# Optimization experiments

Measured on AMD Instinct MI355X. Metric: run time of the kernel, lower is better.

The kernel has to match this reference:

```python
import jax, jax.numpy as jnp
import numpy as np

HEADS = 8
DIM_HEAD = 64
BOTTLENECK = 40


def setup_inputs() -> dict:
    key = jax.random.key(0)
    ks = jax.random.split(key, 10)
    b, n, qs = 4, 1024, 256
    inner = HEADS * DIM_HEAD
    s = lambda fan_in: 1.0 / np.sqrt(fan_in)
    return {
        "x":   jax.random.normal(ks[0], (b, n, qs), dtype=jnp.float32),
        # weights stored as (in, out) so forward is x @ W
        "wq1": jax.random.normal(ks[1], (qs, BOTTLENECK), dtype=jnp.float32) * s(qs),
        "wq2": jax.random.normal(ks[2], (BOTTLENECK, inner), dtype=jnp.float32) * s(BOTTLENECK),
        "wk1": jax.random.normal(ks[3], (qs, BOTTLENECK), dtype=jnp.float32) * s(qs),
        "wk2": jax.random.normal(ks[4], (BOTTLENECK, inner), dtype=jnp.float32) * s(BOTTLENECK),
        "wv1": jax.random.normal(ks[5], (qs, BOTTLENECK), dtype=jnp.float32) * s(qs),
        "wv2": jax.random.normal(ks[6], (BOTTLENECK, inner), dtype=jnp.float32) * s(BOTTLENECK),
        "wo":  jax.random.normal(ks[7], (inner, qs), dtype=jnp.float32) * s(inner),
        "bo":  jax.random.normal(ks[8], (qs,), dtype=jnp.float32) * 0.01,
    }


def reference(x, wq1, wq2, wk1, wk2, wv1, wv2, wo, bo):
    b, n, _ = x.shape
    h, d = HEADS, DIM_HEAD
    scale = d ** -0.5

    # bottlenecked QKV projections (40-dim), SiLU on K bottleneck
    q = (x @ wq1) @ wq2                       # (b, n, h*d)
    k = jax.nn.silu(x @ wk1) @ wk2            # (b, n, h*d)
    v = (x @ wv1) @ wv2                       # (b, n, h*d)

    def split(t):  # 'b n (h d) -> b (h n) d'
        return t.reshape(b, n, h, d).transpose(0, 2, 1, 3).reshape(b, h * n, d)

    q, k, v = split(q), split(k), split(v)

    sim = jnp.einsum('bid,bjd->bij', q, k) * scale   # (b, h*n, h*n)
    attn = jax.nn.softmax(sim, axis=-1)
    out = jnp.einsum('bij,bjd->bid', attn, v)        # (b, h*n, d)

    # 'b (h n) d -> b n (h d)'
    out = out.reshape(b, h, n, d).transpose(0, 2, 1, 3).reshape(b, n, h * d)
    return out @ wo + bo
```

## Files before the change

### kernel.cpp

```cpp
#include <hip/hip_runtime.h>
#include <hip/hip_bf16.h>


#define B_    4
#define H_    8
#define NSEQ  1024
#define SEQ   8192
#define DH    64
#define QS    256
#define INNER 512
#define QSCALE 0.18033688011112042f

#define KVSW_BATCH 524288

typedef __bf16 bf16x8 __attribute__((ext_vector_type(8)));
typedef float floatx4 __attribute__((ext_vector_type(4)));

__global__ __launch_bounds__(1024) void qkv_kernel(
    const float* __restrict__ x,
    const float* __restrict__ wq1, const float* __restrict__ wq2,
    const float* __restrict__ wk1, const float* __restrict__ wk2,
    const float* __restrict__ wv1, const float* __restrict__ wv2,
    __hip_bfloat16* __restrict__ Qg, __hip_bfloat16* __restrict__ KSg,
    __hip_bfloat16* __restrict__ VSg)
{
  const int tid  = threadIdx.x;
  const int b    = blockIdx.x >> 6;
  const int nblk = blockIdx.x & 63;
  const int n0   = nblk << 4;

  __shared__ __align__(16) float xs[16][260];
  __shared__ __align__(16) float tb2[2][3][16][40];
  __shared__ __align__(16) float tb[3][16][40];
  __shared__ __align__(16) __hip_bfloat16 qb[16][520];
  __shared__ __align__(16) __hip_bfloat16 kb[16][520];
  __shared__ __align__(16) __hip_bfloat16 vb[512][20];

  for (int i = tid; i < 16 * 256; i += 1024) {
    const int r = i >> 8, c = i & 255;
    xs[r][c] = x[((size_t)b * NSEQ + n0 + r) * QS + c];
  }
  __syncthreads();

  if (tid < 960) {
    const int ks  = (tid >= 480) ? 1 : 0;
    const int t2  = tid - ks * 480;
    const int p   = t2 / 160;
    const int rem = t2 - p * 160;
    const int r   = rem / 10;
    const int bn  = (rem - r * 10) * 4;
    const float* w1 = (p == 0) ? wq1 : (p == 1) ? wk1 : wv1;
    float a0 = 0.f, a1 = 0.f, a2 = 0.f, a3 = 0.f;
    #pragma unroll 4
    for (int c4 = ks * 32; c4 < ks * 32 + 32; ++c4) {
      const float4 xv = *(const float4*)(&xs[r][c4 * 4]);
      const float4 wa = *(const float4*)(w1 + (c4 * 4 + 0) * 40 + bn);
      const float4 wb = *(const float4*)(w1 + (c4 * 4 + 1) * 40 + bn);
      const float4 wc = *(const float4*)(w1 + (c4 * 4 + 2) * 40 + bn);
      const float4 wd = *(const float4*)(w1 + (c4 * 4 + 3) * 40 + bn);
      a0 += xv.x * wa.x + xv.y * wb.x + xv.z * wc.x + xv.w * wd.x;
      a1 += xv.x * wa.y + xv.y * wb.y + xv.z * wc.y + xv.w * wd.y;
      a2 += xv.x * wa.z + xv.y * wb.z + xv.z * wc.z + xv.w * wd.z;
      a3 += xv.x * wa.w + xv.y * wb.w + xv.z * wc.w + xv.w * wd.w;
    }
    tb2[ks][p][r][bn + 0] = a0; tb2[ks][p][r][bn + 1] = a1;
    tb2[ks][p][r][bn + 2] = a2; tb2[ks][p][r][bn + 3] = a3;
  }
  __syncthreads();

  if (tid < 480) {
    const int p   = tid / 160;
    const int rem = tid - p * 160;
    const int r   = rem / 10;
    const int bn  = (rem - r * 10) * 4;
    const float4 h0 = *(const float4*)(&tb2[0][p][r][bn]);
    const float4 h1 = *(const float4*)(&tb2[1][p][r][bn]);
    float a0 = h0.x + h1.x, a1 = h0.y + h1.y, a2 = h0.z + h1.z, a3 = h0.w + h1.w;
    if (p == 1) {
      a0 = a0 / (1.f + __expf(-a0));
      a1 = a1 / (1.f + __expf(-a1));
      a2 = a2 / (1.f + __expf(-a2));
      a3 = a3 / (1.f + __expf(-a3));
    }
    tb[p][r][bn + 0] = a0; tb[p][r][bn + 1] = a1;
    tb[p][r][bn + 2] = a2; tb[p][r][bn + 3] = a3;
  }
  __syncthreads();

  #pragma unroll
  for (int pass = 0; pass < 3; ++pass) {
    const int p  = pass;
    const int cq = tid & 127;
    const int rq = (tid >> 7) & 7;
    const int c  = cq * 4, r0 = rq * 2;
    const float* w2 = (p == 0) ? wq2 : (p == 1) ? wk2 : wv2;
    const float scale = (p == 0) ? QSCALE : 1.0f;
    float acc[2][4];
    #pragma unroll
    for (int i = 0; i < 2; ++i)
      #pragma unroll
      for (int j = 0; j < 4; ++j) acc[i][j] = 0.f;

    #pragma unroll 2
    for (int jb = 0; jb < 10; ++jb) {
      const float4 w0 = *(const float4*)(w2 + (jb * 4 + 0) * INNER + c);
      const float4 w1r = *(const float4*)(w2 + (jb * 4 + 1) * INNER + c);
      const float4 w2r = *(const float4*)(w2 + (jb * 4 + 2) * INNER + c);
      const float4 w3 = *(const float4*)(w2 + (jb * 4 + 3) * INNER + c);
      #pragma unroll
      for (int ri = 0; ri < 2; ++ri) {
        const float4 tv = *(const float4*)(&tb[p][r0 + ri][jb * 4]);
        acc[ri][0] += tv.x * w0.x + tv.y * w1r.x + tv.z * w2r.x + tv.w * w3.x;
        acc[ri][1] += tv.x * w0.y + tv.y * w1r.y + tv.z * w2r.y + tv.w * w3.y;
        acc[ri][2] += tv.x * w0.z + tv.y * w1r.z + tv.z * w2r.z + tv.w * w3.z;
        acc[ri][3] += tv.x * w0.w + tv.y * w1r.w + tv.z * w2r.w + tv.w * w3.w;
      }
    }
    #pragma unroll
    for (int ri = 0; ri < 2; ++ri)
      #pragma unroll
      for (int ci = 0; ci < 4; ++ci) {
        const int cc = c + ci;
        const float v = acc[ri][ci] * scale;
        if (p == 0)      qb[r0 + ri][cc] = __float2bfloat16(v);
        else if (p == 1) kb[r0 + ri][cc] = __float2bfloat16(v);
        else             vb[cc][r0 + ri] = __float2bfloat16(v);
      }
  }
  __syncthreads();

  {
    const int i  = tid;
    const int h  = i >> 7;
    const int r  = (i >> 3) & 15;
    const int d8 = i & 7;
    *(float4*)(Qg + ((size_t)b * SEQ + h * NSEQ + n0 + r) * DH + d8 * 8) =
        *(const float4*)(&qb[r][h * 64 + d8 * 8]);
  }

  {
    const int i    = tid;
    const int h    = i >> 7;
    const int ks   = (i >> 6) & 1;
    const int quad = (i >> 4) & 3;
    const int r    = i & 15;
    const int lane = quad * 16 + r;
    const size_t dst = (size_t)b * KVSW_BATCH
        + ((size_t)((h * 64 + nblk) * 2 + ks) * 64 + lane) * 8;
    *(float4*)(KSg + dst) = *(const float4*)(&kb[r][h * 64 + ks * 32 + quad * 8]);
  }

  {
    const int st  = nblk & 1;
    const int p32 = nblk >> 1;
    #pragma unroll
    for (int pass = 0; pass < 2; ++pass) {
      const int i   = tid + pass * 1024;
      const int h   = i >> 8;
      const int dnt = (i >> 6) & 3;
      const int dm  = (i >> 2) & 15;
      const int rg  = i & 3;
      const int lane = rg * 16 + dm;
      const size_t dst = (size_t)b * KVSW_BATCH
          + ((size_t)((h * 32 + p32) * 4 + dnt) * 64 + lane) * 8 + st * 4;
      *(uint2*)(VSg + dst) = *(const uint2*)(&vb[h * 64 + dnt * 16 + dm][rg * 4]);
    }
  }
}

struct PairBuf {
  bf16x8 k[2][2];
  bf16x8 v[4];
};

__global__ __launch_bounds__(256, 3) void attn_kernel(
    const __hip_bfloat16* __restrict__ Qg,
    const __hip_bfloat16* __restrict__ KSg,
    const __hip_bfloat16* __restrict__ VSg,
    float* __restrict__ OPg,
    float* __restrict__ PSg)
{
  __shared__ float Osh[4][16][68];
  __shared__ float psums[4][64];

  const int tid  = threadIdx.x;
  const int wave = tid >> 6;
  const int lane = tid & 63;
  const int lrow = lane & 15;
  const int quad = lane >> 4;

  const int xcd   = blockIdx.x & 7;
  const int idx   = blockIdx.x >> 3;
  const int b     = xcd >> 1;
  const int half  = idx & 1;
  const int qtile = (xcd & 1) * 64 + (idx >> 1);
  const int qbase = qtile * 64;

  const __hip_bfloat16* Qb  = Qg + ((size_t)b * SEQ + qbase) * DH;
  const __hip_bfloat16* kp0 = KSg + (size_t)b * KVSW_BATCH + half * 262144
                              + (size_t)wave * 65536 + lane * 8;
  const __hip_bfloat16* vp0 = VSg + (size_t)b * KVSW_BATCH + half * 262144
                              + (size_t)wave * 65536 + lane * 8;

  bf16x8 qf[4][2];
  #pragma unroll
  for (int mt = 0; mt < 4; ++mt)
    #pragma unroll
    for (int s = 0; s < 2; ++s)
      qf[mt][s] = *(const bf16x8*)(Qb + (mt * 16 + lrow) * DH + s * 32 + quad * 8);

  floatx4 oacc[4][4];
  #pragma unroll
  for (int mt = 0; mt < 4; ++mt)
    #pragma unroll
    for (int dnt = 0; dnt < 4; ++dnt)
      oacc[mt][dnt] = (floatx4){0.f, 0.f, 0.f, 0.f};
  float psum[4] = {0.f, 0.f, 0.f, 0.f};

  #pragma unroll 2
  for (int pair = 0; pair < 32; ++pair) {
    PairBuf pb;
    const __hip_bfloat16* kp = kp0 + pair * 2048;
    pb.k[0][0] = *(const bf16x8*)(kp);
    pb.k[0][1] = *(const bf16x8*)(kp + 512);
    pb.k[1][0] = *(const bf16x8*)(kp + 1024);
    pb.k[1][1] = *(const bf16x8*)(kp + 1536);
    const __hip_bfloat16* vp = vp0 + pair * 2048;
    #pragma unroll
    for (int dnt = 0; dnt < 4; ++dnt)
      pb.v[dnt] = *(const bf16x8*)(vp + dnt * 512);

    #pragma unroll
    for (int mt = 0; mt < 4; ++mt) {
      floatx4 s0 = (floatx4){0.f, 0.f, 0.f, 0.f};
      floatx4 s1 = (floatx4){0.f, 0.f, 0.f, 0.f};
      s0 = __builtin_amdgcn_mfma_f32_16x16x32_bf16(pb.k[0][0], qf[mt][0], s0, 0, 0, 0);
      s0 = __builtin_amdgcn_mfma_f32_16x16x32_bf16(pb.k[0][1], qf[mt][1], s0, 0, 0, 0);
      s1 = __builtin_amdgcn_mfma_f32_16x16x32_bf16(pb.k[1][0], qf[mt][0], s1, 0, 0, 0);
      s1 = __builtin_amdgcn_mfma_f32_16x16x32_bf16(pb.k[1][1], qf[mt][1], s1, 0, 0, 0);
      float p[8];
      #pragma unroll
      for (int r = 0; r < 4; ++r) {
        p[r]     = __builtin_amdgcn_exp2f(s0[r]);
        p[4 + r] = __builtin_amdgcn_exp2f(s1[r]);
      }
      psum[mt] += ((p[0] + p[1]) + (p[2] + p[3])) + ((p[4] + p[5]) + (p[6] + p[7]));
      bf16x8 pa;
      #pragma unroll
      for (int j = 0; j < 8; ++j) pa[j] = (__bf16)p[j];
      #pragma unroll
      for (int dnt = 0; dnt < 4; ++dnt)
        oacc[mt][dnt] = __builtin_amdgcn_mfma_f32_16x16x32_bf16(pa, pb.v[dnt], oacc[mt][dnt], 0, 0, 0);
    }
  }

  #pragma unroll
  for (int mt = 0; mt < 4; ++mt) {
    float s = psum[mt];
    s += __shfl_xor(s, 16, 64);
    s += __shfl_xor(s, 32, 64);
    psum[mt] = s;
  }
  if (quad == 0) {
    #pragma unroll
    for (int mt = 0; mt < 4; ++mt)
      psums[wave][mt * 16 + lrow] = psum[mt];
  }

  const size_t opbase = ((size_t)half * B_ + b) * SEQ + qbase;

  #pragma unroll
  for (int mt = 0; mt < 4; ++mt) {
    #pragma unroll
    for (int dnt = 0; dnt < 4; ++dnt)
      #pragma unroll
      for (int r = 0; r < 4; ++r)
        Osh[wave][quad * 4 + r][dnt * 16 + lrow] = oacc[mt][dnt][r];
    __syncthreads();

    {
      const int q16 = tid >> 4;
      const int d0  = (tid & 15) * 4;
      float4 a0 = *(const float4*)(&Osh[0][q16][d0]);
      float4 a1 = *(const float4*)(&Osh[1][q16][d0]);
      float4 a2 = *(const float4*)(&Osh[2][q16][d0]);
      float4 a3 = *(const float4*)(&Osh[3][q16][d0]);
      float4 res;
      res.x = (a0.x + a1.x) + (a2.x + a3.x);
      res.y = (a0.y + a1.y) + (a2.y + a3.y);
      res.z = (a0.z + a1.z) + (a2.z + a3.z);
      res.w = (a0.w + a1.w) + (a2.w + a3.w);
      *(float4*)(OPg + (opbase + mt * 16 + q16) * DH + d0) = res;
    }
    if (mt == 0 && tid < 64) {
      const float tot = (psums[0][tid] + psums[1][tid]) + (psums[2][tid] + psums[3][tid]);
      PSg[opbase + tid] = tot;
    }
    __syncthreads();
  }
}

__global__ __launch_bounds__(512) void out_kernel(
    const float* __restrict__ OPg, const float* __restrict__ PSg,
    const float* __restrict__ wo, const float* __restrict__ bo,
    float* __restrict__ out)
{
  const int tid = threadIdx.x;
  const int b   = blockIdx.x >> 6;
  const int n0  = (blockIdx.x & 63) << 4;

  __shared__ __align__(16) float os[16][520];
  __shared__ __align__(16) float wot[2][16][260];
  __shared__ float invs[16][8];

  if (tid < 128) {
    const int r = tid >> 3, h = tid & 7;
    const size_t row = (size_t)b * SEQ + h * NSEQ + n0 + r;
    invs[r][h] = 1.0f / (PSg[row] + PSg[(size_t)B_ * SEQ + row]);
  }
  __syncthreads();

  for (int i = tid; i < 2048; i += 512) {
    const int r  = i >> 7;
    const int c4 = (i & 127) * 4;
    const int h  = c4 >> 6;
    const size_t idx = ((size_t)b * SEQ + h * NSEQ + n0 + r) * DH + (c4 & 63);
    const float4 p0 = *(const float4*)(OPg + idx);
    const float4 p1 = *(const float4*)(OPg + (size_t)B_ * SEQ * DH + idx);
    const float inv = invs[r][c4 >> 6];
    float4 m;
    m.x = (p0.x + p1.x) * inv;
    m.y = (p0.y + p1.y) * inv;
    m.z = (p0.z + p1.z) * inv;
    m.w = (p0.w + p1.w) * inv;
    *(float4*)(&os[r][c4]) = m;
  }

  {
    const int c0 = tid, c1 = tid + 512;
    const float4 v0 = *(const float4*)(wo + (size_t)(c0 >> 6) * QS + (c0 & 63) * 4);
    const float4 v1 = *(const float4*)(wo + (size_t)(c1 >> 6) * QS + (c1 & 63) * 4);
    *(float4*)(&wot[0][c0 >> 6][(c0 & 63) * 4]) = v0;
    *(float4*)(&wot[0][c1 >> 6][(c1 & 63) * 4]) = v1;
  }
  __syncthreads();

  const int oq = tid & 63;
  const int rq = tid >> 6;
  const int o  = oq * 4;
  const int r0 = rq * 2;

  float acc[2][4];
  #pragma unroll
  for (int i = 0; i < 2; ++i)
    #pragma unroll
    for (int j = 0; j < 4; ++j) acc[i][j] = 0.f;

  for (int kt = 0; kt < 32; ++kt) {
    const int cur = kt & 1;
    float4 pf0, pf1;
    const int c0 = tid, c1 = tid + 512;
    if (kt < 31) {
      const int kb = (kt + 1) * 16;
      pf0 = *(const float4*)(wo + (size_t)(kb + (c0 >> 6)) * QS + (c0 & 63) * 4);
      pf1 = *(const float4*)(wo + (size_t)(kb + (c1 >> 6)) * QS + (c1 & 63) * 4);
    }

    const int kbase = kt * 16;
    #pragma unroll
    for (int kq = 0; kq < 4; ++kq) {
      const float4 ov0 = *(const float4*)(&os[r0][kbase + kq * 4]);
      const float4 ov1 = *(const float4*)(&os[r0 + 1][kbase + kq * 4]);
      #pragma unroll
      for (int j = 0; j < 4; ++j) {
        const float4 w = *(const float4*)(&wot[cur][kq * 4 + j][o]);
        const float a = (j == 0) ? ov0.x : (j == 1) ? ov0.y : (j == 2) ? ov0.z : ov0.w;
        const float bq = (j == 0) ? ov1.x : (j == 1) ? ov1.y : (j == 2) ? ov1.z : ov1.w;
        acc[0][0] += a * w.x; acc[0][1] += a * w.y;
        acc[0][2] += a * w.z; acc[0][3] += a * w.w;
        acc[1][0] += bq * w.x; acc[1][1] += bq * w.y;
        acc[1][2] += bq * w.z; acc[1][3] += bq * w.w;
      }
    }

    if (kt < 31) {
      *(float4*)(&wot[cur ^ 1][c0 >> 6][(c0 & 63) * 4]) = pf0;
      *(float4*)(&wot[cur ^ 1][c1 >> 6][(c1 & 63) * 4]) = pf1;
    }
    __syncthreads();
  }

  const float4 bv = *(const float4*)(bo + o);
  #pragma unroll
  for (int ri = 0; ri < 2; ++ri) {
    float4 res;
    res.x = acc[ri][0] + bv.x;
    res.y = acc[ri][1] + bv.y;
    res.z = acc[ri][2] + bv.z;
    res.w = acc[ri][3] + bv.w;
    *(float4*)(out + ((size_t)b * NSEQ + n0 + r0 + ri) * QS + o) = res;
  }
}

extern "C" void kernel_launch(void* const* d_in, const int* in_sizes, int n_in,
                              void* d_out, int out_size, void* d_ws, size_t ws_size,
                              hipStream_t stream) {
  const float* x   = (const float*)d_in[0];
  const float* wq1 = (const float*)d_in[1];
  const float* wq2 = (const float*)d_in[2];
  const float* wk1 = (const float*)d_in[3];
  const float* wk2 = (const float*)d_in[4];
  const float* wv1 = (const float*)d_in[5];
  const float* wv2 = (const float*)d_in[6];
  const float* wo  = (const float*)d_in[7];
  const float* bo  = (const float*)d_in[8];
  float* out = (float*)d_out;

  __hip_bfloat16* Qg  = (__hip_bfloat16*)d_ws;
  __hip_bfloat16* KSg = Qg + (size_t)B_ * SEQ * DH;
  __hip_bfloat16* VSg = KSg + (size_t)B_ * KVSW_BATCH;
  float*          OPg = (float*)(VSg + (size_t)B_ * KVSW_BATCH);
  float*          PSg = OPg + 2 * (size_t)B_ * SEQ * DH;

  qkv_kernel<<<256, 1024, 0, stream>>>(x, wq1, wq2, wk1, wk2, wv1, wv2, Qg, KSg, VSg);
  attn_kernel<<<1024, 256, 0, stream>>>(Qg, KSg, VSg, OPg, PSg);
  out_kernel<<<256, 512, 0, stream>>>(OPg, PSg, wo, bo, out);
}
```

Measured before the change: 195.3 us.

## Split QKV kernel per projection, software-pipeline K loads, enlarge out tile

The QKV kernel now launches one block per projection (768 blocks instead of 256), so each block computes a single projection with a 4-way split-K and writes only its own output layout. This raises parallelism but loads and reads x three times. The attention loop gains explicit double-buffered K fragment prefetch and s_setprio around the MFMA groups, aiming to hide load latency behind matrix work. The output kernel goes to 256 threads with each thread computing 4 rows, which gives more register reuse per wo element loaded from shared memory.

```diff
diff --git a/kernel.cpp b/kernel.cpp
--- a/kernel.cpp
+++ b/kernel.cpp
@@ -16,7 +16,7 @@
 typedef __bf16 bf16x8 __attribute__((ext_vector_type(8)));
 typedef float floatx4 __attribute__((ext_vector_type(4)));
 
-__global__ __launch_bounds__(1024) void qkv_kernel(
+__global__ __launch_bounds__(1024, 8) void qkv_kernel(
     const float* __restrict__ x,
     const float* __restrict__ wq1, const float* __restrict__ wq2,
     const float* __restrict__ wk1, const float* __restrict__ wk2,
@@ -25,34 +25,36 @@
     __hip_bfloat16* __restrict__ VSg)
 {
   const int tid  = threadIdx.x;
-  const int b    = blockIdx.x >> 6;
-  const int nblk = blockIdx.x & 63;
+  const int p    = blockIdx.x >> 8;
+  const int rest = blockIdx.x & 255;
+  const int b    = rest >> 6;
+  const int nblk = rest & 63;
   const int n0   = nblk << 4;
 
   __shared__ __align__(16) float xs[16][260];
-  __shared__ __align__(16) float tb2[2][3][16][40];
-  __shared__ __align__(16) float tb[3][16][40];
-  __shared__ __align__(16) __hip_bfloat16 qb[16][520];
-  __shared__ __align__(16) __hip_bfloat16 kb[16][520];
-  __shared__ __align__(16) __hip_bfloat16 vb[512][20];
-
-  for (int i = tid; i < 16 * 256; i += 1024) {
-    const int r = i >> 8, c = i & 255;
-    xs[r][c] = x[((size_t)b * NSEQ + n0 + r) * QS + c];
-  }
-  __syncthreads();
-
-  if (tid < 960) {
-    const int ks  = (tid >= 480) ? 1 : 0;
-    const int t2  = tid - ks * 480;
-    const int p   = t2 / 160;
-    const int rem = t2 - p * 160;
+  __shared__ __align__(16) float tb2[4][16][40];
+  __shared__ __align__(16) float tb[16][40];
+  __shared__ __align__(16) __hip_bfloat16 ob[10400];
+
+  const float* w1 = (p == 0) ? wq1 : (p == 1) ? wk1 : wv1;
+  const float* w2 = (p == 0) ? wq2 : (p == 1) ? wk2 : wv2;
+
+  {
+    const int r  = tid >> 6;
+    const int c4 = (tid & 63) << 2;
+    *(float4*)(&xs[r][c4]) =
+        *(const float4*)(x + ((size_t)b * NSEQ + n0 + r) * QS + c4);
+  }
+  __syncthreads();
+
+  if (tid < 640) {
+    const int ks  = tid / 160;
+    const int rem = tid - ks * 160;
     const int r   = rem / 10;
     const int bn  = (rem - r * 10) * 4;
-    const float* w1 = (p == 0) ? wq1 : (p == 1) ? wk1 : wv1;
     float a0 = 0.f, a1 = 0.f, a2 = 0.f, a3 = 0.f;
     #pragma unroll 4
-    for (int c4 = ks * 32; c4 < ks * 32 + 32; ++c4) {
+    for (int c4 = ks * 16; c4 < ks * 16 + 16; ++c4) {
       const float4 xv = *(const float4*)(&xs[r][c4 * 4]);
       const float4 wa = *(const float4*)(w1 + (c4 * 4 + 0) * 40 + bn);
       const float4 wb = *(const float4*)(w1 + (c4 * 4 + 1) * 40 + bn);
@@ -63,37 +65,37 @@
       a2 += xv.x * wa.z + xv.y * wb.z + xv.z * wc.z + xv.w * wd.z;
       a3 += xv.x * wa.w + xv.y * wb.w + xv.z * wc.w + xv.w * wd.w;
     }
-    tb2[ks][p][r][bn + 0] = a0; tb2[ks][p][r][bn + 1] = a1;
-    tb2[ks][p][r][bn + 2] = a2; tb2[ks][p][r][bn + 3] = a3;
-  }
-  __syncthreads();
-
-  if (tid < 480) {
-    const int p   = tid / 160;
-    const int rem = tid - p * 160;
-    const int r   = rem / 10;
-    const int bn  = (rem - r * 10) * 4;
-    const float4 h0 = *(const float4*)(&tb2[0][p][r][bn]);
-    const float4 h1 = *(const float4*)(&tb2[1][p][r][bn]);
-    float a0 = h0.x + h1.x, a1 = h0.y + h1.y, a2 = h0.z + h1.z, a3 = h0.w + h1.w;
+    tb2[ks][r][bn + 0] = a0; tb2[ks][r][bn + 1] = a1;
+    tb2[ks][r][bn + 2] = a2; tb2[ks][r][bn + 3] = a3;
+  }
+  __syncthreads();
+
+  if (tid < 160) {
+    const int r  = tid / 10;
+    const int bn = (tid - r * 10) * 4;
+    const float4 h0 = *(const float4*)(&tb2[0][r][bn]);
+    const float4 h1 = *(const float4*)(&tb2[1][r][bn]);
+    const float4 h2 = *(const float4*)(&tb2[2][r][bn]);
+    const float4 h3 = *(const float4*)(&tb2[3][r][bn]);
+    float a0 = (h0.x + h1.x) + (h2.x + h3.x);
+    float a1 = (h0.y + h1.y) + (h2.y + h3.y);
+    float a2 = (h0.z + h1.z) + (h2.z + h3.z);
+    float a3 = (h0.w + h1.w) + (h2.w + h3.w);
     if (p == 1) {
       a0 = a0 / (1.f + __expf(-a0));
       a1 = a1 / (1.f + __expf(-a1));
       a2 = a2 / (1.f + __expf(-a2));
       a3 = a3 / (1.f + __expf(-a3));
     }
-    tb[p][r][bn + 0] = a0; tb[p][r][bn + 1] = a1;
-    tb[p][r][bn + 2] = a2; tb[p][r][bn + 3] = a3;
-  }
-  __syncthreads();
-
-  #pragma unroll
-  for (int pass = 0; pass < 3; ++pass) {
-    const int p  = pass;
+    tb[r][bn + 0] = a0; tb[r][bn + 1] = a1;
+    tb[r][bn + 2] = a2; tb[r][bn + 3] = a3;
+  }
+  __syncthreads();
+
+  {
     const int cq = tid & 127;
     const int rq = (tid >> 7) & 7;
     const int c  = cq * 4, r0 = rq * 2;
-    const float* w2 = (p == 0) ? wq2 : (p == 1) ? wk2 : wv2;
     const float scale = (p == 0) ? QSCALE : 1.0f;
     float acc[2][4];
     #pragma unroll
@@ -103,13 +105,13 @@
 
     #pragma unroll 2
     for (int jb = 0; jb < 10; ++jb) {
-      const float4 w0 = *(const float4*)(w2 + (jb * 4 + 0) * INNER + c);
+      const float4 w0  = *(const float4*)(w2 + (jb * 4 + 0) * INNER + c);
       const float4 w1r = *(const float4*)(w2 + (jb * 4 + 1) * INNER + c);
       const float4 w2r = *(const float4*)(w2 + (jb * 4 + 2) * INNER + c);
-      const float4 w3 = *(const float4*)(w2 + (jb * 4 + 3) * INNER + c);
+      const float4 w3  = *(const float4*)(w2 + (jb * 4 + 3) * INNER + c);
       #pragma unroll
       for (int ri = 0; ri < 2; ++ri) {
-        const float4 tv = *(const float4*)(&tb[p][r0 + ri][jb * 4]);
+        const float4 tv = *(const float4*)(&tb[r0 + ri][jb * 4]);
         acc[ri][0] += tv.x * w0.x + tv.y * w1r.x + tv.z * w2r.x + tv.w * w3.x;
         acc[ri][1] += tv.x * w0.y + tv.y * w1r.y + tv.z * w2r.y + tv.w * w3.y;
         acc[ri][2] += tv.x * w0.z + tv.y * w1r.z + tv.z * w2r.z + tv.w * w3.z;
@@ -122,35 +124,30 @@
       for (int ci = 0; ci < 4; ++ci) {
         const int cc = c + ci;
         const float v = acc[ri][ci] * scale;
-        if (p == 0)      qb[r0 + ri][cc] = __float2bfloat16(v);
-        else if (p == 1) kb[r0 + ri][cc] = __float2bfloat16(v);
-        else             vb[cc][r0 + ri] = __float2bfloat16(v);
+        if (p == 2) ob[cc * 20 + r0 + ri]   = __float2bfloat16(v);
+        else        ob[(r0 + ri) * 520 + cc] = __float2bfloat16(v);
       }
   }
   __syncthreads();
 
-  {
+  if (p == 0) {
     const int i  = tid;
     const int h  = i >> 7;
     const int r  = (i >> 3) & 15;
     const int d8 = i & 7;
     *(float4*)(Qg + ((size_t)b * SEQ + h * NSEQ + n0 + r) * DH + d8 * 8) =
-        *(const float4*)(&qb[r][h * 64 + d8 * 8]);
-  }
-
-  {
+        *(const float4*)(&ob[r * 520 + h * 64 + d8 * 8]);
+  } else if (p == 1) {
     const int i    = tid;
     const int h    = i >> 7;
-    const int ks   = (i >> 6) & 1;
+    const int ks2  = (i >> 6) & 1;
     const int quad = (i >> 4) & 3;
     const int r    = i & 15;
     const int lane = quad * 16 + r;
     const size_t dst = (size_t)b * KVSW_BATCH
-        + ((size_t)((h * 64 + nblk) * 2 + ks) * 64 + lane) * 8;
-    *(float4*)(KSg + dst) = *(const float4*)(&kb[r][h * 64 + ks * 32 + quad * 8]);
-  }
-
-  {
+        + ((size_t)((h * 64 + nblk) * 2 + ks2) * 64 + lane) * 8;
+    *(float4*)(KSg + dst) = *(const float4*)(&ob[r * 520 + h * 64 + ks2 * 32 + quad * 8]);
+  } else {
     const int st  = nblk & 1;
     const int p32 = nblk >> 1;
     #pragma unroll
@@ -163,15 +160,10 @@
       const int lane = rg * 16 + dm;
       const size_t dst = (size_t)b * KVSW_BATCH
           + ((size_t)((h * 32 + p32) * 4 + dnt) * 64 + lane) * 8 + st * 4;
-      *(uint2*)(VSg + dst) = *(const uint2*)(&vb[h * 64 + dnt * 16 + dm][rg * 4]);
+      *(uint2*)(VSg + dst) = *(const uint2*)(&ob[(h * 64 + dnt * 16 + dm) * 20 + rg * 4]);
     }
   }
 }
-
-struct PairBuf {
-  bf16x8 k[2][2];
-  bf16x8 v[4];
-};
 
 __global__ __launch_bounds__(256, 3) void attn_kernel(
     const __hip_bfloat16* __restrict__ Qg,
@@ -217,27 +209,31 @@
       oacc[mt][dnt] = (floatx4){0.f, 0.f, 0.f, 0.f};
   float psum[4] = {0.f, 0.f, 0.f, 0.f};
 
-  #pragma unroll 2
-  for (int pair = 0; pair < 32; ++pair) {
-    PairBuf pb;
-    const __hip_bfloat16* kp = kp0 + pair * 2048;
-    pb.k[0][0] = *(const bf16x8*)(kp);
-    pb.k[0][1] = *(const bf16x8*)(kp + 512);
-    pb.k[1][0] = *(const bf16x8*)(kp + 1024);
-    pb.k[1][1] = *(const bf16x8*)(kp + 1536);
-    const __hip_bfloat16* vp = vp0 + pair * 2048;
+  auto LOADK = [&](bf16x8 (&k)[2][2], int pr) {
+    const __hip_bfloat16* kp = kp0 + (size_t)pr * 2048;
+    k[0][0] = *(const bf16x8*)(kp);
+    k[0][1] = *(const bf16x8*)(kp + 512);
+    k[1][0] = *(const bf16x8*)(kp + 1024);
+    k[1][1] = *(const bf16x8*)(kp + 1536);
+  };
+
+  auto COMPUTE = [&](const bf16x8 (&k)[2][2], int pr) {
+    const __hip_bfloat16* vp = vp0 + (size_t)pr * 2048;
+    bf16x8 v[4];
     #pragma unroll
     for (int dnt = 0; dnt < 4; ++dnt)
-      pb.v[dnt] = *(const bf16x8*)(vp + dnt * 512);
+      v[dnt] = *(const bf16x8*)(vp + dnt * 512);
 
     #pragma unroll
     for (int mt = 0; mt < 4; ++mt) {
       floatx4 s0 = (floatx4){0.f, 0.f, 0.f, 0.f};
       floatx4 s1 = (floatx4){0.f, 0.f, 0.f, 0.f};
-      s0 = __builtin_amdgcn_mfma_f32_16x16x32_bf16(pb.k[0][0], qf[mt][0], s0, 0, 0, 0);
-      s0 = __builtin_amdgcn_mfma_f32_16x16x32_bf16(pb.k[0][1], qf[mt][1], s0, 0, 0, 0);
-      s1 = __builtin_amdgcn_mfma_f32_16x16x32_bf16(pb.k[1][0], qf[mt][0], s1, 0, 0, 0);
-      s1 = __builtin_amdgcn_mfma_f32_16x16x32_bf16(pb.k[1][1], qf[mt][1], s1, 0, 0, 0);
+      __builtin_amdgcn_s_setprio(1);
+      s0 = __builtin_amdgcn_mfma_f32_16x16x32_bf16(k[0][0], qf[mt][0], s0, 0, 0, 0);
+      s0 = __builtin_amdgcn_mfma_f32_16x16x32_bf16(k[0][1], qf[mt][1], s0, 0, 0, 0);
+      s1 = __builtin_amdgcn_mfma_f32_16x16x32_bf16(k[1][0], qf[mt][0], s1, 0, 0, 0);
+      s1 = __builtin_amdgcn_mfma_f32_16x16x32_bf16(k[1][1], qf[mt][1], s1, 0, 0, 0);
+      __builtin_amdgcn_s_setprio(0);
       float p[8];
       #pragma unroll
       for (int r = 0; r < 4; ++r) {
@@ -248,10 +244,22 @@
       bf16x8 pa;
       #pragma unroll
       for (int j = 0; j < 8; ++j) pa[j] = (__bf16)p[j];
+      __builtin_amdgcn_s_setprio(1);
       #pragma unroll
       for (int dnt = 0; dnt < 4; ++dnt)
-        oacc[mt][dnt] = __builtin_amdgcn_mfma_f32_16x16x32_bf16(pa, pb.v[dnt], oacc[mt][dnt], 0, 0, 0);
-    }
+        oacc[mt][dnt] = __builtin_amdgcn_mfma_f32_16x16x32_bf16(pa, v[dnt], oacc[mt][dnt], 0, 0, 0);
+      __builtin_amdgcn_s_setprio(0);
+    }
+  };
+
+  bf16x8 kA[2][2], kB[2][2];
+  LOADK(kA, 0);
+  #pragma unroll 1
+  for (int pair = 0; pair < 32; pair += 2) {
+    LOADK(kB, pair + 1);
+    COMPUTE(kA, pair);
+    LOADK(kA, (pair + 2) & 31);
+    COMPUTE(kB, pair + 1);
   }
 
   #pragma unroll
@@ -300,7 +308,7 @@
   }
 }
 
-__global__ __launch_bounds__(512) void out_kernel(
+__global__ __launch_bounds__(256) void out_kernel(
     const float* __restrict__ OPg, const float* __restrict__ PSg,
     const float* __restrict__ wo, const float* __restrict__ bo,
     float* __restrict__ out)
@@ -320,14 +328,14 @@
   }
   __syncthreads();
 
-  for (int i = tid; i < 2048; i += 512) {
+  for (int i = tid; i < 2048; i += 256) {
     const int r  = i >> 7;
     const int c4 = (i & 127) * 4;
     const int h  = c4 >> 6;
     const size_t idx = ((size_t)b * SEQ + h * NSEQ + n0 + r) * DH + (c4 & 63);
     const float4 p0 = *(const float4*)(OPg + idx);
     const float4 p1 = *(const float4*)(OPg + (size_t)B_ * SEQ * DH + idx);
-    const float inv = invs[r][c4 >> 6];
+    const float inv = invs[r][h];
     float4 m;
     m.x = (p0.x + p1.x) * inv;
     m.y = (p0.y + p1.y) * inv;
@@ -337,62 +345,72 @@
   }
 
   {
-    const int c0 = tid, c1 = tid + 512;
-    const float4 v0 = *(const float4*)(wo + (size_t)(c0 >> 6) * QS + (c0 & 63) * 4);
-    const float4 v1 = *(const float4*)(wo + (size_t)(c1 >> 6) * QS + (c1 & 63) * 4);
-    *(float4*)(&wot[0][c0 >> 6][(c0 & 63) * 4]) = v0;
-    *(float4*)(&wot[0][c1 >> 6][(c1 & 63) * 4]) = v1;
+    #pragma unroll
+    for (int j = 0; j < 4; ++j) {
+      const int cc = tid + j * 256;
+      *(float4*)(&wot[0][cc >> 6][(cc & 63) * 4]) =
+          *(const float4*)(wo + (size_t)(cc >> 6) * QS + (cc & 63) * 4);
+    }
   }
   __syncthreads();
 
   const int oq = tid & 63;
-  const int rq = tid >> 6;
+  const int rg = tid >> 6;
   const int o  = oq * 4;
-  const int r0 = rq * 2;
-
-  float acc[2][4];
-  #pragma unroll
-  for (int i = 0; i < 2; ++i)
+  const int r0 = rg * 4;
+
+  float acc[4][4];
+  #pragma unroll
+  for (int i = 0; i < 4; ++i)
     #pragma unroll
     for (int j = 0; j < 4; ++j) acc[i][j] = 0.f;
 
   for (int kt = 0; kt < 32; ++kt) {
     const int cur = kt & 1;
-    float4 pf0, pf1;
-    const int c0 = tid, c1 = tid + 512;
+    float4 pf0, pf1, pf2, pf3;
     if (kt < 31) {
       const int kb = (kt + 1) * 16;
+      const int c0 = tid, c1 = tid + 256, c2 = tid + 512, c3 = tid + 768;
       pf0 = *(const float4*)(wo + (size_t)(kb + (c0 >> 6)) * QS + (c0 & 63) * 4);
       pf1 = *(const float4*)(wo + (size_t)(kb + (c1 >> 6)) * QS + (c1 & 63) * 4);
+      pf2 = *(const float4*)(wo + (size_t)(kb + (c2 >> 6)) * QS + (c2 & 63) * 4);
+      pf3 = *(const float4*)(wo + (size_t)(kb + (c3 >> 6)) * QS + (c3 & 63) * 4);
     }
 
     const int kbase = kt * 16;
     #pragma unroll
     for (int kq = 0; kq < 4; ++kq) {
-      const float4 ov0 = *(const float4*)(&os[r0][kbase + kq * 4]);
+      const float4 ov0 = *(const float4*)(&os[r0 + 0][kbase + kq * 4]);
       const float4 ov1 = *(const float4*)(&os[r0 + 1][kbase + kq * 4]);
+      const float4 ov2 = *(const float4*)(&os[r0 + 2][kbase + kq * 4]);
+      const float4 ov3 = *(const float4*)(&os[r0 + 3][kbase + kq * 4]);
       #pragma unroll
       for (int j = 0; j < 4; ++j) {
         const float4 w = *(const float4*)(&wot[cur][kq * 4 + j][o]);
-        const float a = (j == 0) ? ov0.x : (j == 1) ? ov0.y : (j == 2) ? ov0.z : ov0.w;
-        const float bq = (j == 0) ? ov1.x : (j == 1) ? ov1.y : (j == 2) ? ov1.z : ov1.w;
-        acc[0][0] += a * w.x; acc[0][1] += a * w.y;
-        acc[0][2] += a * w.z; acc[0][3] += a * w.w;
-        acc[1][0] += bq * w.x; acc[1][1] += bq * w.y;
-        acc[1][2] += bq * w.z; acc[1][3] += bq * w.w;
+        const float a0 = (j == 0) ? ov0.x : (j == 1) ? ov0.y : (j == 2) ? ov0.z : ov0.w;
+        const float a1 = (j == 0) ? ov1.x : (j == 1) ? ov1.y : (j == 2) ? ov1.z : ov1.w;
+        const float a2 = (j == 0) ? ov2.x : (j == 1) ? ov2.y : (j == 2) ? ov2.z : ov2.w;
+        const float a3 = (j == 0) ? ov3.x : (j == 1) ? ov3.y : (j == 2) ? ov3.z : ov3.w;
+        acc[0][0] += a0 * w.x; acc[0][1] += a0 * w.y; acc[0][2] += a0 * w.z; acc[0][3] += a0 * w.w;
+        acc[1][0] += a1 * w.x; acc[1][1] += a1 * w.y; acc[1][2] += a1 * w.z; acc[1][3] += a1 * w.w;
+        acc[2][0] += a2 * w.x; acc[2][1] += a2 * w.y; acc[2][2] += a2 * w.z; acc[2][3] += a2 * w.w;
+        acc[3][0] += a3 * w.x; acc[3][1] += a3 * w.y; acc[3][2] += a3 * w.z; acc[3][3] += a3 * w.w;
       }
     }
 
     if (kt < 31) {
+      const int c0 = tid, c1 = tid + 256, c2 = tid + 512, c3 = tid + 768;
       *(float4*)(&wot[cur ^ 1][c0 >> 6][(c0 & 63) * 4]) = pf0;
       *(float4*)(&wot[cur ^ 1][c1 >> 6][(c1 & 63) * 4]) = pf1;
+      *(float4*)(&wot[cur ^ 1][c2 >> 6][(c2 & 63) * 4]) = pf2;
+      *(float4*)(&wot[cur ^ 1][c3 >> 6][(c3 & 63) * 4]) = pf3;
     }
     __syncthreads();
   }
 
   const float4 bv = *(const float4*)(bo + o);
   #pragma unroll
-  for (int ri = 0; ri < 2; ++ri) {
+  for (int ri = 0; ri < 4; ++ri) {
     float4 res;
     res.x = acc[ri][0] + bv.x;
     res.y = acc[ri][1] + bv.y;
@@ -422,7 +440,7 @@
   float*          OPg = (float*)(VSg + (size_t)B_ * KVSW_BATCH);
   float*          PSg = OPg + 2 * (size_t)B_ * SEQ * DH;
 
-  qkv_kernel<<<256, 1024, 0, stream>>>(x, wq1, wq2, wk1, wk2, wv1, wv2, Qg, KSg, VSg);
+  qkv_kernel<<<768, 1024, 0, stream>>>(x, wq1, wq2, wk1, wk2, wv1, wv2, Qg, KSg, VSg);
   attn_kernel<<<1024, 256, 0, stream>>>(Qg, KSg, VSg, OPg, PSg);
-  out_kernel<<<256, 512, 0, stream>>>(OPg, PSg, wo, bo, out);
+  out_kernel<<<256, 256, 0, stream>>>(OPg, PSg, wo, bo, out);
 }
```

Result: slower. 468.0 us (+139.6%).
